# Optimization experiments

Hardware: AMD Instinct MI355X
Metric: run time of the kernel (lower is better)

The kernel has to match this reference:

```python
import jax, jax.numpy as jnp
import numpy as np

EPS = 1e-5
TEMP = 50.0


def setup_inputs() -> dict:
    key = jax.random.key(0)
    features = jax.random.normal(key, (4, 64, 128, 128), dtype=jnp.float32)
    return {"features": features, "patch_sim_neiref_neisimavgsize": 5}


def reference(features, patch_sim_neiref_neisimavgsize):
    k = patch_sim_neiref_neisimavgsize
    B, C, H, W = features.shape
    pad = k // 2
    xp = jnp.pad(features, ((0, 0), (0, 0), (pad, pad), (pad, pad)))
    # windows ordered (kh, kw) to match F.unfold: [B, k*k, C, H, W]
    wins = jnp.stack([xp[:, :, i:i + H, j:j + W]
                      for i in range(k) for j in range(k)], axis=1)
    # [B, H, W, k*k, C]
    patch = jnp.transpose(wins, (0, 3, 4, 1, 2)) + EPS
    patch_norm = patch / jnp.sqrt(jnp.sum(patch * patch, axis=-1, keepdims=True))
    center = patch_norm[..., (k * k) // 2:(k * k) // 2 + 1, :]  # center pixel of window
    sim = jnp.sum(patch_norm * center, axis=-1, keepdims=True)   # cosine sim [B,H,W,kk,1]
    wei = jax.nn.softmax(TEMP * sim, axis=-2)
    repr_vec = jnp.sum(patch * wei, axis=-2)                     # [B,H,W,C]
    return jnp.transpose(repr_vec, (0, 3, 1, 2))                 # [B,C,H,W]
```

## Files before the change

kernel.cpp:

```cpp
#include <hip/hip_runtime.h>

#define EPS 1e-5f
#define TEMP 50.0f
#define CCH 64
#define HH 128
#define WW 128
#define HWSZ (HH * WW)
#define CEPS2 (CCH * EPS * EPS)
#define K2E 72.13475204444817f

#define IT 8
#define HT 12
#define HPX (HT * HT)
#define HPAD 145

typedef _Float16 h16;
typedef h16 h2v __attribute__((ext_vector_type(2)));
typedef h16 h8v __attribute__((ext_vector_type(8)));
union H8 { h8v v; h2v p[4]; };

__device__ __forceinline__ float fdot2(h2v a, h2v b, float c) {
#if __has_builtin(__builtin_amdgcn_fdot2)
    return __builtin_amdgcn_fdot2(a, b, c, false);
#else
    return c + (float)a[0] * (float)b[0] + (float)a[1] * (float)b[1];
#endif
}

__device__ __forceinline__ h2v pkrtz(float a, float b) {
#if __has_builtin(__builtin_amdgcn_cvt_pkrtz)
    return __builtin_bit_cast(h2v, __builtin_amdgcn_cvt_pkrtz(a, b));
#else
    return (h2v){(h16)a, (h16)b};
#endif
}

__device__ __forceinline__ float fexp2(float x) {
#if __has_builtin(__builtin_amdgcn_exp2f)
    return __builtin_amdgcn_exp2f(x);
#else
    return exp2f(x);
#endif
}

__device__ __forceinline__ float frcp(float x) {
#if __has_builtin(__builtin_amdgcn_rcpf)
    return __builtin_amdgcn_rcpf(x);
#else
    return 1.f / x;
#endif
}

__device__ __forceinline__ float quad_sum(float x) {
#if __has_builtin(__builtin_amdgcn_mov_dpp)
    int i = __builtin_bit_cast(int, x);
    int a = __builtin_amdgcn_mov_dpp(i, 0xB1, 0xF, 0xF, true);
    float x1 = x + __builtin_bit_cast(float, a);
    int j = __builtin_bit_cast(int, x1);
    int b = __builtin_amdgcn_mov_dpp(j, 0x4E, 0xF, 0xF, true);
    return x1 + __builtin_bit_cast(float, b);
#else
    float x1 = x + __shfl_xor(x, 1);
    return x1 + __shfl_xor(x1, 2);
#endif
}

#define TP_PAD 72
__global__ __launch_bounds__(256) void rv_transpose(const float* __restrict__ x,
                                                    h16* __restrict__ xt) {
    __shared__ h16 buf[WW][TP_PAD];
    const int t = threadIdx.x;
    const int h = blockIdx.x;
    const int b = blockIdx.y;
    const float* src = x + (size_t)b * (CCH * HWSZ) + h * WW;
#pragma unroll 4
    for (int i = 0; i < 16; ++i) {
        int k = i * 256 + t;
        int w  = k & 127;
        int cp = k >> 7;
        float v0 = src[(size_t)(2 * cp) * HWSZ + w];
        float v1 = src[(size_t)(2 * cp + 1) * HWSZ + w];
        *(h2v*)&buf[w][2 * cp] = pkrtz(v0, v1);
    }
    __syncthreads();
    h16* dst = xt + (size_t)(b * HH + h) * WW * CCH;
#pragma unroll
    for (int j = 0; j < 4; ++j) {
        int idx = j * 256 + t;
        int w = idx >> 3;
        int q = idx & 7;
        h8v v = *(const h8v*)&buf[w][q * 8];
        *(h8v*)&dst[(size_t)w * CCH + q * 8] = v;
    }
}

__global__ __launch_bounds__(256) void rv_fused(const h16* __restrict__ xt,
                                                float* __restrict__ out) {
    __shared__ h8v  tile[8][HPAD];
    __shared__ float sh_rn[HPX];

    const int t  = threadIdx.x;
    const int w0 = blockIdx.x * IT;
    const int h0 = blockIdx.y * IT;
    const int b  = blockIdx.z;

#pragma unroll
    for (int it = 0; it < 5; ++it) {
        int k = it * 256 + t;
        if (k < 8 * HPX) {
            int q  = k & 7;
            int px = k >> 3;
            int row = px / HT;
            int col = px - row * HT;
            int gh = h0 + row - 2;
            int gw = w0 + col - 2;
            h8v v = {};
            if ((unsigned)gh < (unsigned)HH && (unsigned)gw < (unsigned)WW) {
                v = *(const h8v*)&xt[((size_t)(b * HH + gh) * WW + gw) * CCH + q * 8];
            }
            tile[q][px] = v;
        }
    }
    __syncthreads();

    if (t < HPX) {
        float q = 0.f;
#pragma unroll
        for (int hq = 0; hq < 8; ++hq) {
            H8 u; u.v = tile[hq][t];
#pragma unroll
            for (int j = 0; j < 4; ++j) q = fdot2(u.p[j], u.p[j], q);
        }
        sh_rn[t] = rsqrtf(q + CEPS2);
    }
    __syncthreads();

    const int qg  = t & 3;
    const int pix = t >> 2;
    const int r   = pix >> 3;
    const int cl  = pix & 7;
    const int cpx = (r + 2) * HT + (cl + 2);

    const float rinvC2 = K2E * sh_rn[cpx];

    H8 ctr0, ctr1;
    ctr0.v = tile[2 * qg][cpx];
    ctr1.v = tile[2 * qg + 1][cpx];

    h2v acc[8] = {};
    float wsum = 0.f;

#pragma unroll
    for (int dr = 0; dr < 5; ++dr) {
#pragma unroll
        for (int dc = 0; dc < 5; ++dc) {
            const int npx = (r + dr) * HT + (cl + dc);
            H8 a0, a1;
            a0.v = tile[2 * qg][npx];
            a1.v = tile[2 * qg + 1][npx];
            float d = 0.f;
#pragma unroll
            for (int j = 0; j < 4; ++j) d = fdot2(ctr0.p[j], a0.p[j], d);
#pragma unroll
            for (int j = 0; j < 4; ++j) d = fdot2(ctr1.p[j], a1.p[j], d);
            d = quad_sum(d);
            const float u = (d + CEPS2) * sh_rn[npx];
            const float wn = fexp2(fmaf(u, rinvC2, -K2E));
            wsum += wn;
            const h16 wh = (h16)wn;
            const h2v w2 = {wh, wh};
#pragma unroll
            for (int j = 0; j < 4; ++j) {
                acc[j]     = a0.p[j] * w2 + acc[j];
                acc[4 + j] = a1.p[j] * w2 + acc[4 + j];
            }
        }
    }

    const float rs = frcp(wsum);
    const size_t obase = (size_t)b * (CCH * HWSZ)
                       + (size_t)(qg * 16) * HWSZ
                       + (h0 + r) * WW + (w0 + cl);
#pragma unroll
    for (int j = 0; j < 8; ++j) {
        const float f0 = (float)acc[j][0];
        const float f1 = (float)acc[j][1];
        out[obase + (size_t)(2 * j) * HWSZ]     = fmaf(f0, rs, EPS);
        out[obase + (size_t)(2 * j + 1) * HWSZ] = fmaf(f1, rs, EPS);
    }
}

extern "C" void kernel_launch(void* const* d_in, const int* in_sizes, int n_in,
                              void* d_out, int out_size, void* d_ws, size_t ws_size,
                              hipStream_t stream) {
    const float* x = (const float*)d_in[0];
    float* outp = (float*)d_out;
    h16* xt = (h16*)d_ws;

    rv_transpose<<<dim3(HH, 4), dim3(256), 0, stream>>>(x, xt);
    rv_fused<<<dim3(WW / IT, HH / IT, 4), dim3(256, 1, 1), 0, stream>>>(xt, outp);
}
```

Measured before the change: 80.29 us.

## Fuse NCHW-to-fp16 transpose into main kernel's halo tile load

New measurement: 93.43 us. 16.4% more time.

```diff
diff --git a/kernel.cpp b/kernel.cpp
--- a/kernel.cpp
+++ b/kernel.cpp
@@ -16,8 +16,10 @@
 
 typedef _Float16 h16;
 typedef h16 h2v __attribute__((ext_vector_type(2)));
+typedef h16 h4v __attribute__((ext_vector_type(4)));
 typedef h16 h8v __attribute__((ext_vector_type(8)));
 union H8 { h8v v; h2v p[4]; };
+union H4 { h4v v; h2v p[2]; };
 
 __device__ __forceinline__ float fdot2(h2v a, h2v b, float c) {
 #if __has_builtin(__builtin_amdgcn_fdot2)
@@ -65,37 +67,8 @@
 #endif
 }
 
-#define TP_PAD 72
-__global__ __launch_bounds__(256) void rv_transpose(const float* __restrict__ x,
-                                                    h16* __restrict__ xt) {
-    __shared__ h16 buf[WW][TP_PAD];
-    const int t = threadIdx.x;
-    const int h = blockIdx.x;
-    const int b = blockIdx.y;
-    const float* src = x + (size_t)b * (CCH * HWSZ) + h * WW;
-#pragma unroll 4
-    for (int i = 0; i < 16; ++i) {
-        int k = i * 256 + t;
-        int w  = k & 127;
-        int cp = k >> 7;
-        float v0 = src[(size_t)(2 * cp) * HWSZ + w];
-        float v1 = src[(size_t)(2 * cp + 1) * HWSZ + w];
-        *(h2v*)&buf[w][2 * cp] = pkrtz(v0, v1);
-    }
-    __syncthreads();
-    h16* dst = xt + (size_t)(b * HH + h) * WW * CCH;
-#pragma unroll
-    for (int j = 0; j < 4; ++j) {
-        int idx = j * 256 + t;
-        int w = idx >> 3;
-        int q = idx & 7;
-        h8v v = *(const h8v*)&buf[w][q * 8];
-        *(h8v*)&dst[(size_t)w * CCH + q * 8] = v;
-    }
-}
-
-__global__ __launch_bounds__(256) void rv_fused(const h16* __restrict__ xt,
-                                                float* __restrict__ out) {
+__global__ __launch_bounds__(256) void rv_onepass(const float* __restrict__ x,
+                                                  float* __restrict__ out) {
     __shared__ h8v  tile[8][HPAD];
     __shared__ float sh_rn[HPX];
 
@@ -104,21 +77,30 @@
     const int h0 = blockIdx.y * IT;
     const int b  = blockIdx.z;
 
+    {
+        const int quad = t >> 4;
+        const int l16  = t & 15;
+        const float* s0 = x + ((size_t)b * CCH + 4 * quad) * HWSZ;
+        const float* s1 = s0 + HWSZ;
+        const float* s2 = s1 + HWSZ;
+        const float* s3 = s2 + HWSZ;
+        h16* dst = (h16*)tile + (size_t)(quad >> 1) * (HPAD * 8) + (quad & 1) * 4;
 #pragma unroll
-    for (int it = 0; it < 5; ++it) {
-        int k = it * 256 + t;
-        if (k < 8 * HPX) {
-            int q  = k & 7;
-            int px = k >> 3;
-            int row = px / HT;
-            int col = px - row * HT;
-            int gh = h0 + row - 2;
-            int gw = w0 + col - 2;
-            h8v v = {};
+        for (int s = 0; s < 9; ++s) {
+            const int px  = s * 16 + l16;
+            const int row = px / HT;
+            const int col = px - row * HT;
+            const int gh  = h0 + row - 2;
+            const int gw  = w0 + col - 2;
+            float v0 = 0.f, v1 = 0.f, v2 = 0.f, v3 = 0.f;
             if ((unsigned)gh < (unsigned)HH && (unsigned)gw < (unsigned)WW) {
-                v = *(const h8v*)&xt[((size_t)(b * HH + gh) * WW + gw) * CCH + q * 8];
+                const int off = gh * WW + gw;
+                v0 = s0[off]; v1 = s1[off]; v2 = s2[off]; v3 = s3[off];
             }
-            tile[q][px] = v;
+            H4 u;
+            u.p[0] = pkrtz(v0, v1);
+            u.p[1] = pkrtz(v2, v3);
+            *(h4v*)(dst + px * 8) = u.v;
         }
     }
     __syncthreads();
@@ -195,8 +177,7 @@
                               hipStream_t stream) {
     const float* x = (const float*)d_in[0];
     float* outp = (float*)d_out;
-    h16* xt = (h16*)d_ws;
+    (void)d_ws; (void)ws_size;
 
-    rv_transpose<<<dim3(HH, 4), dim3(256), 0, stream>>>(x, xt);
-    rv_fused<<<dim3(WW / IT, HH / IT, 4), dim3(256, 1, 1), 0, stream>>>(xt, outp);
+    rv_onepass<<<dim3(WW / IT, HH / IT, 4), dim3(256, 1, 1), 0, stream>>>(x, outp);
 }
```

## Widen fused tile to 16x8 with 512 threads and split norm pass

Applied to the files above, without the earlier changes.

After: 79.51 us. Within noise of the previous version (-1.0%).

```diff
diff --git a/kernel.cpp b/kernel.cpp
--- a/kernel.cpp
+++ b/kernel.cpp
@@ -9,10 +9,12 @@
 #define CEPS2 (CCH * EPS * EPS)
 #define K2E 72.13475204444817f
 
-#define IT 8
-#define HT 12
-#define HPX (HT * HT)
-#define HPAD 145
+#define ITW 16
+#define ITH 8
+#define HTW 20
+#define HTH 12
+#define HPX (HTW * HTH)
+#define HPAD 241
 
 typedef _Float16 h16;
 typedef h16 h2v __attribute__((ext_vector_type(2)));
@@ -51,11 +53,19 @@
 #endif
 }
 
-__device__ __forceinline__ float quad_sum(float x) {
+__device__ __forceinline__ float dpp_xor1(float x) {
 #if __has_builtin(__builtin_amdgcn_mov_dpp)
     int i = __builtin_bit_cast(int, x);
     int a = __builtin_amdgcn_mov_dpp(i, 0xB1, 0xF, 0xF, true);
-    float x1 = x + __builtin_bit_cast(float, a);
+    return __builtin_bit_cast(float, a);
+#else
+    return __shfl_xor(x, 1);
+#endif
+}
+
+__device__ __forceinline__ float quad_sum(float x) {
+#if __has_builtin(__builtin_amdgcn_mov_dpp)
+    float x1 = x + dpp_xor1(x);
     int j = __builtin_bit_cast(int, x1);
     int b = __builtin_amdgcn_mov_dpp(j, 0x4E, 0xF, 0xF, true);
     return x1 + __builtin_bit_cast(float, b);
@@ -94,24 +104,24 @@
     }
 }
 
-__global__ __launch_bounds__(256) void rv_fused(const h16* __restrict__ xt,
+__global__ __launch_bounds__(512) void rv_fused(const h16* __restrict__ xt,
                                                 float* __restrict__ out) {
     __shared__ h8v  tile[8][HPAD];
     __shared__ float sh_rn[HPX];
 
     const int t  = threadIdx.x;
-    const int w0 = blockIdx.x * IT;
-    const int h0 = blockIdx.y * IT;
+    const int w0 = blockIdx.x * ITW;
+    const int h0 = blockIdx.y * ITH;
     const int b  = blockIdx.z;
 
 #pragma unroll
-    for (int it = 0; it < 5; ++it) {
-        int k = it * 256 + t;
+    for (int it = 0; it < 4; ++it) {
+        int k = it * 512 + t;
         if (k < 8 * HPX) {
             int q  = k & 7;
             int px = k >> 3;
-            int row = px / HT;
-            int col = px - row * HT;
+            int row = px / HTW;
+            int col = px - row * HTW;
             int gh = h0 + row - 2;
             int gw = w0 + col - 2;
             h8v v = {};
@@ -123,23 +133,26 @@
     }
     __syncthreads();
 
-    if (t < HPX) {
+    if (t < 2 * HPX) {
+        const int px   = t >> 1;
+        const int hbse = (t & 1) * 4;
         float q = 0.f;
 #pragma unroll
-        for (int hq = 0; hq < 8; ++hq) {
-            H8 u; u.v = tile[hq][t];
+        for (int hq = 0; hq < 4; ++hq) {
+            H8 u; u.v = tile[hbse + hq][px];
 #pragma unroll
             for (int j = 0; j < 4; ++j) q = fdot2(u.p[j], u.p[j], q);
         }
-        sh_rn[t] = rsqrtf(q + CEPS2);
+        const float qt = q + dpp_xor1(q);
+        if (!(t & 1)) sh_rn[px] = rsqrtf(qt + CEPS2);
     }
     __syncthreads();
 
     const int qg  = t & 3;
     const int pix = t >> 2;
-    const int r   = pix >> 3;
-    const int cl  = pix & 7;
-    const int cpx = (r + 2) * HT + (cl + 2);
+    const int r   = pix >> 4;
+    const int cl  = pix & 15;
+    const int cpx = (r + 2) * HTW + (cl + 2);
 
     const float rinvC2 = K2E * sh_rn[cpx];
 
@@ -154,16 +167,16 @@
     for (int dr = 0; dr < 5; ++dr) {
 #pragma unroll
         for (int dc = 0; dc < 5; ++dc) {
-            const int npx = (r + dr) * HT + (cl + dc);
+            const int npx = (r + dr) * HTW + (cl + dc);
             H8 a0, a1;
             a0.v = tile[2 * qg][npx];
             a1.v = tile[2 * qg + 1][npx];
-            float d = 0.f;
-#pragma unroll
-            for (int j = 0; j < 4; ++j) d = fdot2(ctr0.p[j], a0.p[j], d);
-#pragma unroll
-            for (int j = 0; j < 4; ++j) d = fdot2(ctr1.p[j], a1.p[j], d);
-            d = quad_sum(d);
+            float d0 = 0.f, d1 = 0.f;
+#pragma unroll
+            for (int j = 0; j < 4; ++j) d0 = fdot2(ctr0.p[j], a0.p[j], d0);
+#pragma unroll
+            for (int j = 0; j < 4; ++j) d1 = fdot2(ctr1.p[j], a1.p[j], d1);
+            float d = quad_sum(d0 + d1);
             const float u = (d + CEPS2) * sh_rn[npx];
             const float wn = fexp2(fmaf(u, rinvC2, -K2E));
             wsum += wn;
@@ -198,5 +211,5 @@
     h16* xt = (h16*)d_ws;
 
     rv_transpose<<<dim3(HH, 4), dim3(256), 0, stream>>>(x, xt);
-    rv_fused<<<dim3(WW / IT, HH / IT, 4), dim3(256, 1, 1), 0, stream>>>(xt, outp);
-}
+    rv_fused<<<dim3(WW / ITW, HH / ITH, 4), dim3(512, 1, 1), 0, stream>>>(xt, outp);
+}
```
